# Kernel tuning notes

Measured on AMD Instinct MI355X. Metric: run time of the kernel, lower is better.

The kernel has to match this reference:

```python
import jax, jax.numpy as jnp
import numpy as np

T, F, H = 91, 256, 4
D = F // H  # 64
KF = 4 * F  # FFN hidden
A, R = 128, 1024


def setup_inputs() -> dict:
    key = jax.random.key(0)
    ks = jax.random.split(key, 16)
    s = 1.0 / np.sqrt(F)
    inp = {
        "agent": jax.random.normal(ks[0], (A, T, F), jnp.float32),
        "rg": jax.random.normal(ks[1], (R, T, F), jnp.float32),
        "W_K": jax.random.uniform(ks[2], (F, F), jnp.float32, -s, s),
        "b_K": jnp.zeros((F,), jnp.float32),
        "W_V": jax.random.uniform(ks[3], (F, F), jnp.float32, -s, s),
        "b_V": jnp.zeros((F,), jnp.float32),
        "W_Q": jax.random.uniform(ks[4], (F, F), jnp.float32, -s, s),
        "b_Q": jnp.zeros((F,), jnp.float32),
        "q_scale": jnp.full((D,), 1e-3, jnp.float32),  # ScaleLayer init_value
        "W_Y2": jax.random.uniform(ks[5], (F, F), jnp.float32, -s, s),
        "b_Y2": jnp.zeros((F,), jnp.float32),
        "W_F1": jax.random.uniform(ks[6], (F, KF), jnp.float32, -s, s),
        "b_F1": jnp.zeros((KF,), jnp.float32),
        "W_F2": jax.random.uniform(ks[7], (KF, F), jnp.float32, -1.0 / np.sqrt(KF), 1.0 / np.sqrt(KF)),
        "b_F2": jnp.zeros((F,), jnp.float32),
        "ln_g": jnp.ones((F,), jnp.float32),
        "ln_b": jnp.zeros((F,), jnp.float32),
    }
    return inp


def _proj_heads(x, W, b):
    # Linear + ReLU + View(-1, T, H, D) + permute(1,2,0,3) -> [T, H, N, D]
    y = jax.nn.relu(x @ W + b)                      # [N, T, F]
    y = y.reshape(-1, T, H, D)
    return jnp.transpose(y, (1, 2, 0, 3))            # [T, H, N, D]


def _layernorm(x, g, b, eps=1e-5):
    mu = jnp.mean(x, axis=-1, keepdims=True)
    var = jnp.var(x, axis=-1, keepdims=True)
    return (x - mu) * jax.lax.rsqrt(var + eps) * g + b


def reference(agent, rg, W_K, b_K, W_V, b_V, W_Q, b_Q, q_scale,
              W_Y2, b_Y2, W_F1, b_F1, W_F2, b_F2, ln_g, ln_b):
    Kh = _proj_heads(rg, W_K, b_K)                   # [T, H, R, D]
    Vh = _proj_heads(rg, W_V, b_V)                   # [T, H, R, D]
    Qh = _proj_heads(agent, W_Q, b_Q) * q_scale      # [T, H, A, D] (per-channel scale)

    scale = jnp.sqrt(jnp.asarray(float(H), jnp.float32))  # sqrt(head_num), as in source
    energy = jnp.einsum('thad,thrd->thar', Qh, Kh) / scale
    attn = jax.nn.softmax(energy, axis=-1)           # [T, H, A, R]
    Y1 = jnp.einsum('thar,thrd->thad', attn, Vh)     # [T, H, A, D]
    Y1 = jnp.transpose(Y1, (2, 0, 1, 3)).reshape(-1, T, F)  # [A, T, F]

    Y2 = jax.nn.relu(Y1 @ W_Y2 + b_Y2)               # [A, T, F]
    S = Y2 + agent
    F1 = jax.nn.relu(S @ W_F1 + b_F1)                # [A, T, 4F]
    F2 = jax.nn.relu(F1 @ W_F2 + b_F2)               # [A, T, F]
    Z = _layernorm(F2, ln_g, ln_b)
    return (Z, Qh, Kh, Vh)
```

## Files before the change

### kernel.cpp

```cpp
#include <hip/hip_runtime.h>

#define T91  91
#define FDIM 256
#define HNUM 4
#define DDIM 64
#define ANUM 128
#define RNUM 1024
#define KFDIM 1024

typedef __attribute__((ext_vector_type(8))) short short8v;
typedef __attribute__((ext_vector_type(4))) float f32x4;

__device__ __forceinline__ ushort f2bf(float f) {
  union { float f; uint32_t u; } c; c.f = f;
  return (ushort)((c.u + 0x7FFFu + ((c.u >> 16) & 1u)) >> 16);
}
__device__ __forceinline__ short8v pack8(float4 a, float4 b) {
  short8v v;
  v[0] = (short)f2bf(a.x); v[1] = (short)f2bf(a.y);
  v[2] = (short)f2bf(a.z); v[3] = (short)f2bf(a.w);
  v[4] = (short)f2bf(b.x); v[5] = (short)f2bf(b.y);
  v[6] = (short)f2bf(b.z); v[7] = (short)f2bf(b.w);
  return v;
}

__global__ __launch_bounds__(256) void wconv(
    const float* __restrict__ W, ushort* __restrict__ Wt, int Kd, int Md, int total) {
  const int o = blockIdx.x * 256 + threadIdx.x;
  if (o >= total) return;
  const int m = o / Kd, k = o - m * Kd;
  Wt[o] = f2bf(W[(size_t)k * Md + m]);
}

template<int ISV>
__global__ __launch_bounds__(256) void kvproj_mfma(
    const float* __restrict__ rg, const ushort* __restrict__ Wt,
    const float* __restrict__ bias, float* __restrict__ outKV,
    ushort* __restrict__ Vt) {
  const int rt = blockIdx.x;
  const int tfix = blockIdx.y;
  const int tid = threadIdx.x;
  const int wid = tid >> 6, lane = tid & 63, lg = lane >> 4, li = lane & 15;

  __shared__ ushort As[64 * 64];
  __shared__ ushort Bs[256 * 64];

  const int r0 = rt * 64;
  const int ar = tid >> 2, aseg = (tid & 3) * 16;
  const float* arow = rg + ((size_t)(r0 + ar) * T91 + tfix) * FDIM;

  f32x4 acc[4][4];
  #pragma unroll
  for (int a = 0; a < 4; ++a)
    #pragma unroll
    for (int b = 0; b < 4; ++b)
      #pragma unroll
      for (int i = 0; i < 4; ++i) acc[a][b][i] = 0.f;

  for (int ks = 0; ks < 4; ++ks) {
    const int k0 = ks * 64;
    float4 a0 = *(const float4*)&arow[k0 + aseg + 0];
    float4 a1 = *(const float4*)&arow[k0 + aseg + 4];
    float4 a2 = *(const float4*)&arow[k0 + aseg + 8];
    float4 a3 = *(const float4*)&arow[k0 + aseg + 12];
    short8v bv[8];
    #pragma unroll
    for (int j = 0; j < 8; ++j)
      bv[j] = *(const short8v*)&Wt[(size_t)tid * 256 + k0 + j * 8];
    __syncthreads();
    {
      const int sw = (ar & 7) << 4;
      const int ab = ar * 128 + (tid & 3) * 32;
      *(short8v*)((char*)As + ((ab + 0) ^ sw)) = pack8(a0, a1);
      *(short8v*)((char*)As + ((ab + 16) ^ sw)) = pack8(a2, a3);
      const int swb = (tid & 7) << 4;
      #pragma unroll
      for (int j = 0; j < 8; ++j)
        *(short8v*)((char*)Bs + (tid * 128 + ((j * 16) ^ swb))) = bv[j];
    }
    __syncthreads();
    #pragma unroll
    for (int kc = 0; kc < 2; ++kc) {
      short8v af[4], bfr[4];
      #pragma unroll
      for (int ms = 0; ms < 4; ++ms) {
        const int r = ms * 16 + li;
        af[ms] = *(const short8v*)((char*)As + ((r * 128 + kc * 64 + lg * 16) ^ ((r & 7) << 4)));
      }
      #pragma unroll
      for (int ns = 0; ns < 4; ++ns) {
        const int n = wid * 64 + ns * 16 + li;
        bfr[ns] = *(const short8v*)((char*)Bs + ((n * 128 + kc * 64 + lg * 16) ^ ((n & 7) << 4)));
      }
      #pragma unroll
      for (int ms = 0; ms < 4; ++ms)
        #pragma unroll
        for (int ns = 0; ns < 4; ++ns)
          acc[ms][ns] = __builtin_amdgcn_mfma_f32_16x16x32_bf16(af[ms], bfr[ns], acc[ms][ns], 0, 0, 0);
    }
  }

  const int th = tfix * HNUM + wid;
  float* kout = outKV + (size_t)th * RNUM * DDIM;
  #pragma unroll
  for (int ns = 0; ns < 4; ++ns) {
    const int d = ns * 16 + li;
    const float bb = bias[wid * 64 + d];
    #pragma unroll
    for (int ms = 0; ms < 4; ++ms) {
      float v[4];
      #pragma unroll
      for (int i = 0; i < 4; ++i) {
        v[i] = fmaxf(acc[ms][ns][i] + bb, 0.f);
        kout[(size_t)(r0 + ms * 16 + lg * 4 + i) * DDIM + d] = v[i];
      }
      if (ISV) {
        ushort4 u = {f2bf(v[0]), f2bf(v[1]), f2bf(v[2]), f2bf(v[3])};
        *(ushort4*)&Vt[((size_t)(th * 16 + rt) * 64 + d) * 64 + ms * 16 + lg * 4] = u;
      }
    }
  }
}

template<int MODE>
__global__ __launch_bounds__(256) void mfma_gemm(
    const float* __restrict__ A, const ushort* __restrict__ Wt,
    const float* __restrict__ bias, float* __restrict__ out,
    const float* __restrict__ aux) {
  const int n0 = blockIdx.y * 64;
  const int m0 = blockIdx.x * 256;
  const int tid = threadIdx.x;
  const int wid = tid >> 6, lane = tid & 63, lg = lane >> 4, li = lane & 15;

  __shared__ ushort As[64 * 64];
  __shared__ ushort Bs[256 * 64];

  const int ar = tid >> 2, aseg = (tid & 3) * 16;
  const float* arow = A + (size_t)(n0 + ar) * 256;

  f32x4 acc[4][4];
  #pragma unroll
  for (int a = 0; a < 4; ++a)
    #pragma unroll
    for (int b = 0; b < 4; ++b)
      #pragma unroll
      for (int i = 0; i < 4; ++i) acc[a][b][i] = 0.f;

  for (int ks = 0; ks < 4; ++ks) {
    const int k0 = ks * 64;
    float4 a0 = *(const float4*)&arow[k0 + aseg + 0];
    float4 a1 = *(const float4*)&arow[k0 + aseg + 4];
    float4 a2 = *(const float4*)&arow[k0 + aseg + 8];
    float4 a3 = *(const float4*)&arow[k0 + aseg + 12];
    short8v bv[8];
    #pragma unroll
    for (int j = 0; j < 8; ++j)
      bv[j] = *(const short8v*)&Wt[(size_t)(m0 + tid) * 256 + k0 + j * 8];
    __syncthreads();
    {
      const int sw = (ar & 7) << 4;
      const int ab = ar * 128 + (tid & 3) * 32;
      *(short8v*)((char*)As + ((ab + 0) ^ sw)) = pack8(a0, a1);
      *(short8v*)((char*)As + ((ab + 16) ^ sw)) = pack8(a2, a3);
      const int swb = (tid & 7) << 4;
      #pragma unroll
      for (int j = 0; j < 8; ++j)
        *(short8v*)((char*)Bs + (tid * 128 + ((j * 16) ^ swb))) = bv[j];
    }
    __syncthreads();
    #pragma unroll
    for (int kc = 0; kc < 2; ++kc) {
      short8v af[4], bfr[4];
      #pragma unroll
      for (int ms = 0; ms < 4; ++ms) {
        const int r = ms * 16 + li;
        af[ms] = *(const short8v*)((char*)As + ((r * 128 + kc * 64 + lg * 16) ^ ((r & 7) << 4)));
      }
      #pragma unroll
      for (int ns = 0; ns < 4; ++ns) {
        const int n = wid * 64 + ns * 16 + li;
        bfr[ns] = *(const short8v*)((char*)Bs + ((n * 128 + kc * 64 + lg * 16) ^ ((n & 7) << 4)));
      }
      #pragma unroll
      for (int ms = 0; ms < 4; ++ms)
        #pragma unroll
        for (int ns = 0; ns < 4; ++ns)
          acc[ms][ns] = __builtin_amdgcn_mfma_f32_16x16x32_bf16(af[ms], bfr[ns], acc[ms][ns], 0, 0, 0);
    }
  }

  #pragma unroll
  for (int ns = 0; ns < 4; ++ns) {
    const int c = wid * 64 + ns * 16 + li;
    const float bb = bias[m0 + c];
    float qs = 0.f;
    if (MODE == 0) qs = aux[c & 63];
    #pragma unroll
    for (int ms = 0; ms < 4; ++ms) {
      #pragma unroll
      for (int i = 0; i < 4; ++i) {
        const int n = n0 + ms * 16 + lg * 4 + i;
        float v = fmaxf(acc[ms][ns][i] + bb, 0.f);
        if (MODE == 0) {
          const int a = n / T91, t = n - a * T91;
          out[(((size_t)t * HNUM + (c >> 6)) * ANUM + a) * DDIM + (c & 63)] = v * qs;
        } else if (MODE == 1) {
          out[(size_t)n * FDIM + c] = v + aux[(size_t)n * FDIM + c];
        } else {
          ((ushort*)out)[(size_t)n * KFDIM + m0 + c] = f2bf(v);
        }
      }
    }
  }
}

__global__ __launch_bounds__(512) void f2_ln_mfma(
    const ushort* __restrict__ F1b, const ushort* __restrict__ Wt,
    const float* __restrict__ b2, const float* __restrict__ g,
    const float* __restrict__ bb, float* __restrict__ Z) {
  const int n0 = blockIdx.x * 64;
  const int tid = threadIdx.x;
  const int wid = tid >> 6, lane = tid & 63, lg = lane >> 4, li = lane & 15;

  __shared__ ushort As[64 * 64];
  __shared__ ushort Bs[256 * 64];
  __shared__ float red[64][8][2];

  const int ar = tid >> 3, aseg = tid & 7;
  const int br = tid >> 1, bh = tid & 1;

  f32x4 acc[4][2];
  #pragma unroll
  for (int a = 0; a < 4; ++a)
    #pragma unroll
    for (int b = 0; b < 2; ++b)
      #pragma unroll
      for (int i = 0; i < 4; ++i) acc[a][b][i] = 0.f;

  for (int ks = 0; ks < 16; ++ks) {
    const int k0 = ks * 64;
    short8v av = *(const short8v*)&F1b[(size_t)(n0 + ar) * KFDIM + k0 + aseg * 8];
    short8v bv[4];
    #pragma unroll
    for (int j = 0; j < 4; ++j)
      bv[j] = *(const short8v*)&Wt[(size_t)br * KFDIM + k0 + bh * 32 + j * 8];
    __syncthreads();
    *(short8v*)((char*)As + (ar * 128 + ((aseg * 16) ^ ((ar & 7) << 4)))) = av;
    #pragma unroll
    for (int j = 0; j < 4; ++j)
      *(short8v*)((char*)Bs + (br * 128 + ((bh * 64 + j * 16) ^ ((br & 7) << 4)))) = bv[j];
    __syncthreads();
    #pragma unroll
    for (int kc = 0; kc < 2; ++kc) {
      short8v af[4], bfr[2];
      #pragma unroll
      for (int ms = 0; ms < 4; ++ms) {
        const int r = ms * 16 + li;
        af[ms] = *(const short8v*)((char*)As + ((r * 128 + kc * 64 + lg * 16) ^ ((r & 7) << 4)));
      }
      #pragma unroll
      for (int ns = 0; ns < 2; ++ns) {
        const int n = wid * 32 + ns * 16 + li;
        bfr[ns] = *(const short8v*)((char*)Bs + ((n * 128 + kc * 64 + lg * 16) ^ ((n & 7) << 4)));
      }
      #pragma unroll
      for (int ms = 0; ms < 4; ++ms)
        #pragma unroll
        for (int ns = 0; ns < 2; ++ns)
          acc[ms][ns] = __builtin_amdgcn_mfma_f32_16x16x32_bf16(af[ms], bfr[ns], acc[ms][ns], 0, 0, 0);
    }
  }

  #pragma unroll
  for (int ms = 0; ms < 4; ++ms) {
    #pragma unroll
    for (int i = 0; i < 4; ++i) {
      float s = 0.f, sq = 0.f;
      #pragma unroll
      for (int ns = 0; ns < 2; ++ns) {
        const float b = b2[wid * 32 + ns * 16 + li];
        float v = fmaxf(acc[ms][ns][i] + b, 0.f);
        acc[ms][ns][i] = v;
        s += v; sq += v * v;
      }
      s += __shfl_xor(s, 1); sq += __shfl_xor(sq, 1);
      s += __shfl_xor(s, 2); sq += __shfl_xor(sq, 2);
      s += __shfl_xor(s, 4); sq += __shfl_xor(sq, 4);
      s += __shfl_xor(s, 8); sq += __shfl_xor(sq, 8);
      if (li == 0) {
        const int r = ms * 16 + lg * 4 + i;
        red[r][wid][0] = s; red[r][wid][1] = sq;
      }
    }
  }
  __syncthreads();

  const float g0 = g[wid * 32 + li],       g1 = g[wid * 32 + 16 + li];
  const float e0 = bb[wid * 32 + li],      e1 = bb[wid * 32 + 16 + li];
  #pragma unroll
  for (int ms = 0; ms < 4; ++ms) {
    #pragma unroll
    for (int i = 0; i < 4; ++i) {
      const int r = ms * 16 + lg * 4 + i;
      float s = 0.f, sq = 0.f;
      #pragma unroll
      for (int w = 0; w < 8; ++w) { s += red[r][w][0]; sq += red[r][w][1]; }
      const float mu = s * (1.f / 256.f);
      const float var = sq * (1.f / 256.f) - mu * mu;
      const float rs = rsqrtf(var + 1e-5f);
      float* zp = Z + (size_t)(n0 + r) * FDIM;
      zp[wid * 32 + li]      = (acc[ms][0][i] - mu) * rs * g0 + e0;
      zp[wid * 32 + 16 + li] = (acc[ms][1][i] - mu) * rs * g1 + e1;
    }
  }
}

__global__ __launch_bounds__(256) void attn_mfma(
    const float* __restrict__ Qh, const float* __restrict__ Kh,
    const ushort* __restrict__ Vt, float* __restrict__ Pacc,
    float* __restrict__ Pml) {
  const int th = blockIdx.x, g = blockIdx.y;
  const int tid = threadIdx.x;
  const int wid = tid >> 6, lane = tid & 63;
  const int lg = lane >> 4, li = lane & 15;

  __shared__ ushort Kl[4096];
  __shared__ ushort Vl[4096];
  __shared__ ushort Pl[8192];

  short8v qf[2][2];
  #pragma unroll
  for (int qsub = 0; qsub < 2; ++qsub)
    #pragma unroll
    for (int kc = 0; kc < 2; ++kc) {
      const float* qp = Qh + ((size_t)th * ANUM + wid * 32 + qsub * 16 + li) * DDIM + kc * 32 + lg * 8;
      float4 x = *(const float4*)qp;
      float4 y = *(const float4*)(qp + 4);
      qf[qsub][kc] = pack8(make_float4(x.x*0.5f, x.y*0.5f, x.z*0.5f, x.w*0.5f),
                           make_float4(y.x*0.5f, y.y*0.5f, y.z*0.5f, y.w*0.5f));
    }

  f32x4 yacc[2][4];
  #pragma unroll
  for (int a = 0; a < 2; ++a)
    #pragma unroll
    for (int b = 0; b < 4; ++b)
      #pragma unroll
      for (int i = 0; i < 4; ++i) yacc[a][b][i] = 0.f;

  float mrow[2][4], lrow[2][4];
  #pragma unroll
  for (int a = 0; a < 2; ++a)
    #pragma unroll
    for (int i = 0; i < 4; ++i) { mrow[a][i] = -1e30f; lrow[a][i] = 0.f; }

  const float*  Kb = Kh + (size_t)th * RNUM * DDIM;
  const ushort* Vb = Vt + (size_t)th * 16 * 4096;

  const int krr = wid * 16 + (lane >> 2);
  const int kd0 = (lane & 3) * 16;

  for (int tt = 0; tt < 8; ++tt) {
    const int r0 = g * 512 + tt * 64;
    const int rt = g * 8 + tt;
    __syncthreads();
    {
      const float* kp = Kb + (size_t)(r0 + krr) * DDIM + kd0;
      float4 a = *(const float4*)kp,       b = *(const float4*)(kp + 4),
             c = *(const float4*)(kp + 8), d = *(const float4*)(kp + 12);
      const int base = krr * 128 + kd0 * 2;
      const int sw = (krr & 7) << 4;
      *(short8v*)((char*)Kl + (base ^ sw)) = pack8(a, b);
      *(short8v*)((char*)Kl + ((base + 16) ^ sw)) = pack8(c, d);
    }
    const ushort* vtile = Vb + rt * 4096;
    #pragma unroll
    for (int c = 0; c < 2; ++c) {
      const int B = (wid * 2 + c) * 1024 + lane * 16;
      const int sw = ((B >> 7) & 7) << 4;
      short8v v = *(const short8v*)((const char*)vtile + (B ^ sw));
      *(short8v*)((char*)Vl + B) = v;
    }
    __syncthreads();

    f32x4 sf[2][4];
    #pragma unroll
    for (int a = 0; a < 2; ++a)
      #pragma unroll
      for (int b = 0; b < 4; ++b)
        #pragma unroll
        for (int i = 0; i < 4; ++i) sf[a][b][i] = 0.f;

    #pragma unroll
    for (int kc = 0; kc < 2; ++kc) {
      short8v kf[4];
      #pragma unroll
      for (int rsub = 0; rsub < 4; ++rsub) {
        const int rl = rsub * 16 + li;
        kf[rsub] = *(const short8v*)((char*)Kl + ((rl * 128 + kc * 64 + lg * 16) ^ ((rl & 7) << 4)));
      }
      #pragma unroll
      for (int qsub = 0; qsub < 2; ++qsub)
        #pragma unroll
        for (int rsub = 0; rsub < 4; ++rsub)
          sf[qsub][rsub] = __builtin_amdgcn_mfma_f32_16x16x32_bf16(
              qf[qsub][kc], kf[rsub], sf[qsub][rsub], 0, 0, 0);
    }

    #pragma unroll
    for (int qsub = 0; qsub < 2; ++qsub)
      #pragma unroll
      for (int i = 0; i < 4; ++i) {
        float em = fmaxf(fmaxf(sf[qsub][0][i], sf[qsub][1][i]),
                         fmaxf(sf[qsub][2][i], sf[qsub][3][i]));
        em = fmaxf(em, __shfl_xor(em, 1));
        em = fmaxf(em, __shfl_xor(em, 2));
        em = fmaxf(em, __shfl_xor(em, 4));
        em = fmaxf(em, __shfl_xor(em, 8));
        const float mn = fmaxf(mrow[qsub][i], em);
        const float fs = __expf(mrow[qsub][i] - mn);
        mrow[qsub][i] = mn;
        const float p0 = __expf(sf[qsub][0][i] - mn);
        const float p1 = __expf(sf[qsub][1][i] - mn);
        const float p2 = __expf(sf[qsub][2][i] - mn);
        const float p3 = __expf(sf[qsub][3][i] - mn);
        float rs = p0 + p1 + p2 + p3;
        rs += __shfl_xor(rs, 1);
        rs += __shfl_xor(rs, 2);
        rs += __shfl_xor(rs, 4);
        rs += __shfl_xor(rs, 8);
        lrow[qsub][i] = lrow[qsub][i] * fs + rs;
        #pragma unroll
        for (int dsub = 0; dsub < 4; ++dsub) yacc[qsub][dsub][i] *= fs;
        const int q = qsub * 16 + lg * 4 + i;
        const int sw = (q & 7) << 4;
        char* pb = (char*)Pl + wid * 4096;
        *(ushort*)(pb + ((q * 128 + (0 * 16 + li) * 2) ^ sw)) = f2bf(p0);
        *(ushort*)(pb + ((q * 128 + (1 * 16 + li) * 2) ^ sw)) = f2bf(p1);
        *(ushort*)(pb + ((q * 128 + (2 * 16 + li) * 2) ^ sw)) = f2bf(p2);
        *(ushort*)(pb + ((q * 128 + (3 * 16 + li) * 2) ^ sw)) = f2bf(p3);
      }

    #pragma unroll
    for (int rc = 0; rc < 2; ++rc) {
      short8v pa[2];
      #pragma unroll
      for (int qsub = 0; qsub < 2; ++qsub) {
        const int qq = qsub * 16 + li;
        pa[qsub] = *(const short8v*)((char*)Pl + wid * 4096 +
                    ((qq * 128 + rc * 64 + lg * 16) ^ ((qq & 7) << 4)));
      }
      #pragma unroll
      for (int dsub = 0; dsub < 4; ++dsub) {
        const int dd = dsub * 16 + li;
        short8v vb = *(const short8v*)((char*)Vl +
                      ((dd * 128 + rc * 64 + lg * 16) ^ ((dd & 7) << 4)));
        #pragma unroll
        for (int qsub = 0; qsub < 2; ++qsub)
          yacc[qsub][dsub] = __builtin_amdgcn_mfma_f32_16x16x32_bf16(
              pa[qsub], vb, yacc[qsub][dsub], 0, 0, 0);
      }
    }
  }

  const int thg = th * 2 + g;
  float* pp = Pacc + (size_t)thg * 8192;
  #pragma unroll
  for (int qsub = 0; qsub < 2; ++qsub)
    #pragma unroll
    for (int dsub = 0; dsub < 4; ++dsub)
      #pragma unroll
      for (int i = 0; i < 4; ++i) {
        const int q = wid * 32 + qsub * 16 + lg * 4 + i;
        pp[q * 64 + dsub * 16 + li] = yacc[qsub][dsub][i];
      }
  if (li == 0) {
    #pragma unroll
    for (int qsub = 0; qsub < 2; ++qsub)
      #pragma unroll
      for (int i = 0; i < 4; ++i) {
        const int q = wid * 32 + qsub * 16 + lg * 4 + i;
        Pml[(size_t)thg * 256 + q] = mrow[qsub][i];
        Pml[(size_t)thg * 256 + 128 + q] = lrow[qsub][i];
      }
  }
}

__global__ __launch_bounds__(128) void attn_combine(
    const float* __restrict__ Pacc, const float* __restrict__ Pml,
    float* __restrict__ Y1) {
  const int th = blockIdx.x;
  const int t = th >> 2, h = th & 3;
  const int a = threadIdx.x;
  const float m0 = Pml[(size_t)(th * 2 + 0) * 256 + a];
  const float l0 = Pml[(size_t)(th * 2 + 0) * 256 + 128 + a];
  const float m1 = Pml[(size_t)(th * 2 + 1) * 256 + a];
  const float l1 = Pml[(size_t)(th * 2 + 1) * 256 + 128 + a];
  const float mn = fmaxf(m0, m1);
  const float s0 = __expf(m0 - mn), s1 = __expf(m1 - mn);
  const float inv = 1.f / (s0 * l0 + s1 * l1);
  const float* p0 = Pacc + (size_t)(th * 2 + 0) * 8192 + a * 64;
  const float* p1 = Pacc + (size_t)(th * 2 + 1) * 8192 + a * 64;
  float* yp = Y1 + ((size_t)a * T91 + t) * FDIM + h * DDIM;
  #pragma unroll
  for (int i = 0; i < 16; ++i) {
    float4 v0 = *(const float4*)(p0 + i * 4);
    float4 v1 = *(const float4*)(p1 + i * 4);
    float4 o = {(s0 * v0.x + s1 * v1.x) * inv, (s0 * v0.y + s1 * v1.y) * inv,
                (s0 * v0.z + s1 * v1.z) * inv, (s0 * v0.w + s1 * v1.w) * inv};
    *(float4*)(yp + i * 4) = o;
  }
}

extern "C" void kernel_launch(void* const* d_in, const int* in_sizes, int n_in,
                              void* d_out, int out_size, void* d_ws, size_t ws_size,
                              hipStream_t stream) {
  (void)in_sizes; (void)n_in; (void)out_size; (void)ws_size;

  const float* agent   = (const float*)d_in[0];
  const float* rg      = (const float*)d_in[1];
  const float* W_K     = (const float*)d_in[2];
  const float* b_K     = (const float*)d_in[3];
  const float* W_V     = (const float*)d_in[4];
  const float* b_V     = (const float*)d_in[5];
  const float* W_Q     = (const float*)d_in[6];
  const float* b_Q     = (const float*)d_in[7];
  const float* q_scale = (const float*)d_in[8];
  const float* W_Y2    = (const float*)d_in[9];
  const float* b_Y2    = (const float*)d_in[10];
  const float* W_F1    = (const float*)d_in[11];
  const float* b_F1    = (const float*)d_in[12];
  const float* W_F2    = (const float*)d_in[13];
  const float* b_F2    = (const float*)d_in[14];
  const float* ln_g    = (const float*)d_in[15];
  const float* ln_b    = (const float*)d_in[16];

  float* out = (float*)d_out;
  float* Z  = out;
  float* Qh = out + 2981888;
  float* Kh = out + 5963776;
  float* Vh = out + 29818880;

  char* w = (char*)d_ws;
  ushort* WKt  = (ushort*)w;                    w += 65536 * 2;
  ushort* WVt  = (ushort*)w;                    w += 65536 * 2;
  ushort* WQt  = (ushort*)w;                    w += 65536 * 2;
  ushort* WY2t = (ushort*)w;                    w += 65536 * 2;
  ushort* WF1t = (ushort*)w;                    w += 262144 * 2;
  ushort* WF2t = (ushort*)w;                    w += 262144 * 2;
  float*  S    = (float*)w;                     w += (size_t)11648 * 256 * 4;
  ushort* F1b  = (ushort*)w;                    w += (size_t)11648 * 1024 * 2;
  ushort* Vt   = (ushort*)w;
  float*  Y1   = (float*)Vt;
  float*  Pacc = (float*)F1b;
  float*  Pml  = S;

  const dim3 blk(256);

  wconv<<<dim3(256), blk, 0, stream>>>(W_K,  WKt,  256, 256, 65536);
  wconv<<<dim3(256), blk, 0, stream>>>(W_V,  WVt,  256, 256, 65536);
  wconv<<<dim3(256), blk, 0, stream>>>(W_Q,  WQt,  256, 256, 65536);
  wconv<<<dim3(256), blk, 0, stream>>>(W_Y2, WY2t, 256, 256, 65536);
  wconv<<<dim3(1024), blk, 0, stream>>>(W_F1, WF1t, 256, 1024, 262144);
  wconv<<<dim3(1024), blk, 0, stream>>>(W_F2, WF2t, 1024, 256, 262144);

  kvproj_mfma<0><<<dim3(16, 91), blk, 0, stream>>>(rg, WKt, b_K, Kh, nullptr);
  kvproj_mfma<1><<<dim3(16, 91), blk, 0, stream>>>(rg, WVt, b_V, Vh, Vt);
  mfma_gemm<0><<<dim3(1, 182), blk, 0, stream>>>(agent, WQt, b_Q, Qh, q_scale);

  attn_mfma<<<dim3(364, 2), blk, 0, stream>>>(Qh, Kh, Vt, Pacc, Pml);
  attn_combine<<<dim3(364), dim3(128), 0, stream>>>(Pacc, Pml, Y1);

  mfma_gemm<1><<<dim3(1, 182), blk, 0, stream>>>(Y1, WY2t, b_Y2, S, agent);
  mfma_gemm<2><<<dim3(4, 182), blk, 0, stream>>>(S, WF1t, b_F1, (float*)F1b, nullptr);
  f2_ln_mfma<<<dim3(182), dim3(512), 0, stream>>>(F1b, WF2t, b_F2, ln_g, ln_b, Z);
}
```

Measured before the change: 557.0 us.

## Fuse weight conversions, K/V projections, and attention combine into Y2 GEMM

Merges the six weight-conversion launches into one kernel and fuses the K and V projections into a single 512-thread kernel, so each rg tile is loaded once for both. Removes the attn_combine kernel and the Y1 round trip by having the Y2 GEMM merge the two attention partials (m/l rescaling) while loading its A tile. Computes attention scores transposed so each lane owns one query row, which turns most cross-lane softmax shuffles into in-register reductions, and packs P to bf16 with v_cvt_pk_bf16_f32. The fused K/V kernel uses more LDS and threads per block, which may lower occupancy, and Pml moves to its own workspace region.

```diff
diff --git a/kernel.cpp b/kernel.cpp
--- a/kernel.cpp
+++ b/kernel.cpp
@@ -23,31 +23,53 @@
   v[6] = (short)f2bf(b.z); v[7] = (short)f2bf(b.w);
   return v;
 }
-
-__global__ __launch_bounds__(256) void wconv(
-    const float* __restrict__ W, ushort* __restrict__ Wt, int Kd, int Md, int total) {
-  const int o = blockIdx.x * 256 + threadIdx.x;
-  if (o >= total) return;
+__device__ __forceinline__ uint32_t cvtpk(float lo, float hi) {
+  uint32_t r;
+  asm("v_cvt_pk_bf16_f32 %0, %1, %2" : "=v"(r) : "v"(lo), "v"(hi));
+  return r;
+}
+
+__global__ __launch_bounds__(256) void wconv_all(
+    const float* __restrict__ W_K, const float* __restrict__ W_V,
+    const float* __restrict__ W_Q, const float* __restrict__ W_Y2,
+    const float* __restrict__ W_F1, const float* __restrict__ W_F2,
+    ushort* __restrict__ WKt, ushort* __restrict__ WVt,
+    ushort* __restrict__ WQt, ushort* __restrict__ WY2t,
+    ushort* __restrict__ WF1t, ushort* __restrict__ WF2t) {
+  const int b = blockIdx.x, tid = threadIdx.x;
+  const float* W; ushort* Wt; int Kd, Md, o;
+  if (b < 1024) {
+    const int s = b >> 8;
+    W  = (s == 0) ? W_K : (s == 1) ? W_V : (s == 2) ? W_Q : W_Y2;
+    Wt = (s == 0) ? WKt : (s == 1) ? WVt : (s == 2) ? WQt : WY2t;
+    Kd = 256; Md = 256; o = (b & 255) * 256 + tid;
+  } else if (b < 2048) {
+    W = W_F1; Wt = WF1t; Kd = 256; Md = 1024; o = (b - 1024) * 256 + tid;
+  } else {
+    W = W_F2; Wt = WF2t; Kd = 1024; Md = 256; o = (b - 2048) * 256 + tid;
+  }
   const int m = o / Kd, k = o - m * Kd;
   Wt[o] = f2bf(W[(size_t)k * Md + m]);
 }
 
-template<int ISV>
-__global__ __launch_bounds__(256) void kvproj_mfma(
-    const float* __restrict__ rg, const ushort* __restrict__ Wt,
-    const float* __restrict__ bias, float* __restrict__ outKV,
-    ushort* __restrict__ Vt) {
+__global__ __launch_bounds__(512) void kvproj_fused(
+    const float* __restrict__ rg, const ushort* __restrict__ WKt,
+    const ushort* __restrict__ WVt, const float* __restrict__ b_K,
+    const float* __restrict__ b_V, float* __restrict__ Kh,
+    float* __restrict__ Vh, ushort* __restrict__ Vt) {
   const int rt = blockIdx.x;
   const int tfix = blockIdx.y;
   const int tid = threadIdx.x;
   const int wid = tid >> 6, lane = tid & 63, lg = lane >> 4, li = lane & 15;
 
   __shared__ ushort As[64 * 64];
-  __shared__ ushort Bs[256 * 64];
+  __shared__ ushort Bs[512 * 64];
 
   const int r0 = rt * 64;
-  const int ar = tid >> 2, aseg = (tid & 3) * 16;
+  const int ar = tid >> 3, aseg = (tid & 7) * 8;
   const float* arow = rg + ((size_t)(r0 + ar) * T91 + tfix) * FDIM;
+  const ushort* brow = (tid < 256) ? (WKt + (size_t)tid * 256)
+                                   : (WVt + (size_t)(tid - 256) * 256);
 
   f32x4 acc[4][4];
   #pragma unroll
@@ -61,18 +83,14 @@
     const int k0 = ks * 64;
     float4 a0 = *(const float4*)&arow[k0 + aseg + 0];
     float4 a1 = *(const float4*)&arow[k0 + aseg + 4];
-    float4 a2 = *(const float4*)&arow[k0 + aseg + 8];
-    float4 a3 = *(const float4*)&arow[k0 + aseg + 12];
     short8v bv[8];
     #pragma unroll
     for (int j = 0; j < 8; ++j)
-      bv[j] = *(const short8v*)&Wt[(size_t)tid * 256 + k0 + j * 8];
+      bv[j] = *(const short8v*)&brow[k0 + j * 8];
     __syncthreads();
     {
       const int sw = (ar & 7) << 4;
-      const int ab = ar * 128 + (tid & 3) * 32;
-      *(short8v*)((char*)As + ((ab + 0) ^ sw)) = pack8(a0, a1);
-      *(short8v*)((char*)As + ((ab + 16) ^ sw)) = pack8(a2, a3);
+      *(short8v*)((char*)As + (ar * 128 + (((tid & 7) * 16) ^ sw))) = pack8(a0, a1);
       const int swb = (tid & 7) << 4;
       #pragma unroll
       for (int j = 0; j < 8; ++j)
@@ -100,12 +118,15 @@
     }
   }
 
-  const int th = tfix * HNUM + wid;
-  float* kout = outKV + (size_t)th * RNUM * DDIM;
+  const int hsel = wid & 3;
+  const int th = tfix * HNUM + hsel;
+  const bool isv = wid >= 4;
+  const float* bias = isv ? b_V : b_K;
+  float* kout = (isv ? Vh : Kh) + (size_t)th * RNUM * DDIM;
   #pragma unroll
   for (int ns = 0; ns < 4; ++ns) {
     const int d = ns * 16 + li;
-    const float bb = bias[wid * 64 + d];
+    const float bb = bias[hsel * 64 + d];
     #pragma unroll
     for (int ms = 0; ms < 4; ++ms) {
       float v[4];
@@ -114,7 +135,7 @@
         v[i] = fmaxf(acc[ms][ns][i] + bb, 0.f);
         kout[(size_t)(r0 + ms * 16 + lg * 4 + i) * DDIM + d] = v[i];
       }
-      if (ISV) {
+      if (isv) {
         ushort4 u = {f2bf(v[0]), f2bf(v[1]), f2bf(v[2]), f2bf(v[3])};
         *(ushort4*)&Vt[((size_t)(th * 16 + rt) * 64 + d) * 64 + ms * 16 + lg * 4] = u;
       }
@@ -204,11 +225,105 @@
         if (MODE == 0) {
           const int a = n / T91, t = n - a * T91;
           out[(((size_t)t * HNUM + (c >> 6)) * ANUM + a) * DDIM + (c & 63)] = v * qs;
-        } else if (MODE == 1) {
-          out[(size_t)n * FDIM + c] = v + aux[(size_t)n * FDIM + c];
         } else {
           ((ushort*)out)[(size_t)n * KFDIM + m0 + c] = f2bf(v);
         }
+      }
+    }
+  }
+}
+
+__global__ __launch_bounds__(256) void y2_gemm(
+    const float* __restrict__ Pacc, const float* __restrict__ Pml,
+    const ushort* __restrict__ Wt, const float* __restrict__ bias,
+    float* __restrict__ S, const float* __restrict__ agent) {
+  const int n0 = blockIdx.x * 64;
+  const int tid = threadIdx.x;
+  const int wid = tid >> 6, lane = tid & 63, lg = lane >> 4, li = lane & 15;
+
+  __shared__ ushort As[64 * 64];
+  __shared__ ushort Bs[256 * 64];
+
+  const int ar = tid >> 2, aseg = (tid & 3) * 16;
+  const int n = n0 + ar;
+  const int a = n / T91, t = n - a * T91;
+
+  f32x4 acc[4][4];
+  #pragma unroll
+  for (int q = 0; q < 4; ++q)
+    #pragma unroll
+    for (int b = 0; b < 4; ++b)
+      #pragma unroll
+      for (int i = 0; i < 4; ++i) acc[q][b][i] = 0.f;
+
+  for (int ks = 0; ks < 4; ++ks) {
+    const int k0 = ks * 64;
+    const int th = t * 4 + ks;
+    const float m0v = Pml[(size_t)(th * 2 + 0) * 256 + a];
+    const float l0v = Pml[(size_t)(th * 2 + 0) * 256 + 128 + a];
+    const float m1v = Pml[(size_t)(th * 2 + 1) * 256 + a];
+    const float l1v = Pml[(size_t)(th * 2 + 1) * 256 + 128 + a];
+    const float mn = fmaxf(m0v, m1v);
+    const float s0 = __expf(m0v - mn), s1 = __expf(m1v - mn);
+    const float inv = 1.f / (s0 * l0v + s1 * l1v);
+    const float* p0 = Pacc + (size_t)(th * 2 + 0) * 8192 + a * 64 + aseg;
+    const float* p1 = Pacc + (size_t)(th * 2 + 1) * 8192 + a * 64 + aseg;
+    float4 x[4];
+    #pragma unroll
+    for (int j = 0; j < 4; ++j) {
+      float4 u = *(const float4*)(p0 + j * 4);
+      float4 v = *(const float4*)(p1 + j * 4);
+      x[j] = make_float4((s0 * u.x + s1 * v.x) * inv, (s0 * u.y + s1 * v.y) * inv,
+                         (s0 * u.z + s1 * v.z) * inv, (s0 * u.w + s1 * v.w) * inv);
+    }
+    short8v bv[8];
+    #pragma unroll
+    for (int j = 0; j < 8; ++j)
+      bv[j] = *(const short8v*)&Wt[(size_t)tid * 256 + k0 + j * 8];
+    __syncthreads();
+    {
+      const int sw = (ar & 7) << 4;
+      const int ab = ar * 128 + (tid & 3) * 32;
+      *(short8v*)((char*)As + ((ab + 0) ^ sw)) = pack8(x[0], x[1]);
+      *(short8v*)((char*)As + ((ab + 16) ^ sw)) = pack8(x[2], x[3]);
+      const int swb = (tid & 7) << 4;
+      #pragma unroll
+      for (int j = 0; j < 8; ++j)
+        *(short8v*)((char*)Bs + (tid * 128 + ((j * 16) ^ swb))) = bv[j];
+    }
+    __syncthreads();
+    #pragma unroll
+    for (int kc = 0; kc < 2; ++kc) {
+      short8v af[4], bfr[4];
+      #pragma unroll
+      for (int ms = 0; ms < 4; ++ms) {
+        const int r = ms * 16 + li;
+        af[ms] = *(const short8v*)((char*)As + ((r * 128 + kc * 64 + lg * 16) ^ ((r & 7) << 4)));
+      }
+      #pragma unroll
+      for (int ns = 0; ns < 4; ++ns) {
+        const int nn = wid * 64 + ns * 16 + li;
+        bfr[ns] = *(const short8v*)((char*)Bs + ((nn * 128 + kc * 64 + lg * 16) ^ ((nn & 7) << 4)));
+      }
+      #pragma unroll
+      for (int ms = 0; ms < 4; ++ms)
+        #pragma unroll
+        for (int ns = 0; ns < 4; ++ns)
+          acc[ms][ns] = __builtin_amdgcn_mfma_f32_16x16x32_bf16(af[ms], bfr[ns], acc[ms][ns], 0, 0, 0);
+    }
+  }
+
+  #pragma unroll
+  for (int ns = 0; ns < 4; ++ns) {
+    const int c = wid * 64 + ns * 16 + li;
+    const float bb = bias[c];
+    #pragma unroll
+    for (int ms = 0; ms < 4; ++ms) {
+      #pragma unroll
+      for (int i = 0; i < 4; ++i) {
+        const int nn = n0 + ms * 16 + lg * 4 + i;
+        float v = fmaxf(acc[ms][ns][i] + bb, 0.f);
+        S[(size_t)nn * FDIM + c] = v + agent[(size_t)nn * FDIM + c];
       }
     }
   }
@@ -340,19 +455,15 @@
                            make_float4(y.x*0.5f, y.y*0.5f, y.z*0.5f, y.w*0.5f));
     }
 
-  f32x4 yacc[2][4];
+  f32x4 yaccT[2][4];
   #pragma unroll
   for (int a = 0; a < 2; ++a)
     #pragma unroll
     for (int b = 0; b < 4; ++b)
       #pragma unroll
-      for (int i = 0; i < 4; ++i) yacc[a][b][i] = 0.f;
-
-  float mrow[2][4], lrow[2][4];
-  #pragma unroll
-  for (int a = 0; a < 2; ++a)
-    #pragma unroll
-    for (int i = 0; i < 4; ++i) { mrow[a][i] = -1e30f; lrow[a][i] = 0.f; }
+      for (int i = 0; i < 4; ++i) yaccT[a][b][i] = 0.f;
+
+  float mq[2] = {-1e30f, -1e30f}, lq[2] = {0.f, 0.f};
 
   const float*  Kb = Kh + (size_t)th * RNUM * DDIM;
   const ushort* Vb = Vt + (size_t)th * 16 * 4096;
@@ -383,13 +494,13 @@
     }
     __syncthreads();
 
-    f32x4 sf[2][4];
+    f32x4 sfT[2][4];
     #pragma unroll
     for (int a = 0; a < 2; ++a)
       #pragma unroll
       for (int b = 0; b < 4; ++b)
         #pragma unroll
-        for (int i = 0; i < 4; ++i) sf[a][b][i] = 0.f;
+        for (int i = 0; i < 4; ++i) sfT[a][b][i] = 0.f;
 
     #pragma unroll
     for (int kc = 0; kc < 2; ++kc) {
@@ -403,52 +514,58 @@
       for (int qsub = 0; qsub < 2; ++qsub)
         #pragma unroll
         for (int rsub = 0; rsub < 4; ++rsub)
-          sf[qsub][rsub] = __builtin_amdgcn_mfma_f32_16x16x32_bf16(
-              qf[qsub][kc], kf[rsub], sf[qsub][rsub], 0, 0, 0);
-    }
-
-    #pragma unroll
-    for (int qsub = 0; qsub < 2; ++qsub)
-      #pragma unroll
-      for (int i = 0; i < 4; ++i) {
-        float em = fmaxf(fmaxf(sf[qsub][0][i], sf[qsub][1][i]),
-                         fmaxf(sf[qsub][2][i], sf[qsub][3][i]));
-        em = fmaxf(em, __shfl_xor(em, 1));
-        em = fmaxf(em, __shfl_xor(em, 2));
-        em = fmaxf(em, __shfl_xor(em, 4));
-        em = fmaxf(em, __shfl_xor(em, 8));
-        const float mn = fmaxf(mrow[qsub][i], em);
-        const float fs = __expf(mrow[qsub][i] - mn);
-        mrow[qsub][i] = mn;
-        const float p0 = __expf(sf[qsub][0][i] - mn);
-        const float p1 = __expf(sf[qsub][1][i] - mn);
-        const float p2 = __expf(sf[qsub][2][i] - mn);
-        const float p3 = __expf(sf[qsub][3][i] - mn);
-        float rs = p0 + p1 + p2 + p3;
-        rs += __shfl_xor(rs, 1);
-        rs += __shfl_xor(rs, 2);
-        rs += __shfl_xor(rs, 4);
-        rs += __shfl_xor(rs, 8);
-        lrow[qsub][i] = lrow[qsub][i] * fs + rs;
-        #pragma unroll
-        for (int dsub = 0; dsub < 4; ++dsub) yacc[qsub][dsub][i] *= fs;
-        const int q = qsub * 16 + lg * 4 + i;
-        const int sw = (q & 7) << 4;
-        char* pb = (char*)Pl + wid * 4096;
-        *(ushort*)(pb + ((q * 128 + (0 * 16 + li) * 2) ^ sw)) = f2bf(p0);
-        *(ushort*)(pb + ((q * 128 + (1 * 16 + li) * 2) ^ sw)) = f2bf(p1);
-        *(ushort*)(pb + ((q * 128 + (2 * 16 + li) * 2) ^ sw)) = f2bf(p2);
-        *(ushort*)(pb + ((q * 128 + (3 * 16 + li) * 2) ^ sw)) = f2bf(p3);
-      }
+          sfT[qsub][rsub] = __builtin_amdgcn_mfma_f32_16x16x32_bf16(
+              kf[rsub], qf[qsub][kc], sfT[qsub][rsub], 0, 0, 0);
+    }
+
+    #pragma unroll
+    for (int qsub = 0; qsub < 2; ++qsub) {
+      float em = sfT[qsub][0][0];
+      #pragma unroll
+      for (int rsub = 0; rsub < 4; ++rsub)
+        #pragma unroll
+        for (int i = 0; i < 4; ++i)
+          em = fmaxf(em, sfT[qsub][rsub][i]);
+      em = fmaxf(em, __shfl_xor(em, 16));
+      em = fmaxf(em, __shfl_xor(em, 32));
+      const float mn = fmaxf(mq[qsub], em);
+      const float fs = __expf(mq[qsub] - mn);
+      mq[qsub] = mn;
+      float rs = 0.f;
+      #pragma unroll
+      for (int rsub = 0; rsub < 4; ++rsub)
+        #pragma unroll
+        for (int i = 0; i < 4; ++i) {
+          const float p = __expf(sfT[qsub][rsub][i] - mn);
+          sfT[qsub][rsub][i] = p;
+          rs += p;
+        }
+      rs += __shfl_xor(rs, 16);
+      rs += __shfl_xor(rs, 32);
+      lq[qsub] = lq[qsub] * fs + rs;
+      #pragma unroll
+      for (int dsub = 0; dsub < 4; ++dsub)
+        #pragma unroll
+        for (int i = 0; i < 4; ++i) yaccT[qsub][dsub][i] *= fs;
+      const int qloc = qsub * 16 + li;
+      const int sw = (qloc & 7) << 4;
+      char* pb = (char*)Pl + wid * 4096;
+      #pragma unroll
+      for (int rsub = 0; rsub < 4; ++rsub) {
+        uint2 cc = {cvtpk(sfT[qsub][rsub][0], sfT[qsub][rsub][1]),
+                    cvtpk(sfT[qsub][rsub][2], sfT[qsub][rsub][3])};
+        *(uint2*)(pb + (qloc * 128 + ((rsub * 32 + lg * 8) ^ sw))) = cc;
+      }
+    }
 
     #pragma unroll
     for (int rc = 0; rc < 2; ++rc) {
-      short8v pa[2];
+      short8v pbf[2];
       #pragma unroll
       for (int qsub = 0; qsub < 2; ++qsub) {
-        const int qq = qsub * 16 + li;
-        pa[qsub] = *(const short8v*)((char*)Pl + wid * 4096 +
-                    ((qq * 128 + rc * 64 + lg * 16) ^ ((qq & 7) << 4)));
+        const int qloc = qsub * 16 + li;
+        pbf[qsub] = *(const short8v*)((char*)Pl + wid * 4096 +
+                     (qloc * 128 + ((rc * 64 + lg * 16) ^ ((qloc & 7) << 4))));
       }
       #pragma unroll
       for (int dsub = 0; dsub < 4; ++dsub) {
@@ -457,8 +574,8 @@
                       ((dd * 128 + rc * 64 + lg * 16) ^ ((dd & 7) << 4)));
         #pragma unroll
         for (int qsub = 0; qsub < 2; ++qsub)
-          yacc[qsub][dsub] = __builtin_amdgcn_mfma_f32_16x16x32_bf16(
-              pa[qsub], vb, yacc[qsub][dsub], 0, 0, 0);
+          yaccT[qsub][dsub] = __builtin_amdgcn_mfma_f32_16x16x32_bf16(
+              vb, pbf[qsub], yaccT[qsub][dsub], 0, 0, 0);
       }
     }
   }
@@ -466,49 +583,18 @@
   const int thg = th * 2 + g;
   float* pp = Pacc + (size_t)thg * 8192;
   #pragma unroll
-  for (int qsub = 0; qsub < 2; ++qsub)
-    #pragma unroll
-    for (int dsub = 0; dsub < 4; ++dsub)
-      #pragma unroll
-      for (int i = 0; i < 4; ++i) {
-        const int q = wid * 32 + qsub * 16 + lg * 4 + i;
-        pp[q * 64 + dsub * 16 + li] = yacc[qsub][dsub][i];
-      }
-  if (li == 0) {
-    #pragma unroll
-    for (int qsub = 0; qsub < 2; ++qsub)
-      #pragma unroll
-      for (int i = 0; i < 4; ++i) {
-        const int q = wid * 32 + qsub * 16 + lg * 4 + i;
-        Pml[(size_t)thg * 256 + q] = mrow[qsub][i];
-        Pml[(size_t)thg * 256 + 128 + q] = lrow[qsub][i];
-      }
-  }
-}
-
-__global__ __launch_bounds__(128) void attn_combine(
-    const float* __restrict__ Pacc, const float* __restrict__ Pml,
-    float* __restrict__ Y1) {
-  const int th = blockIdx.x;
-  const int t = th >> 2, h = th & 3;
-  const int a = threadIdx.x;
-  const float m0 = Pml[(size_t)(th * 2 + 0) * 256 + a];
-  const float l0 = Pml[(size_t)(th * 2 + 0) * 256 + 128 + a];
-  const float m1 = Pml[(size_t)(th * 2 + 1) * 256 + a];
-  const float l1 = Pml[(size_t)(th * 2 + 1) * 256 + 128 + a];
-  const float mn = fmaxf(m0, m1);
-  const float s0 = __expf(m0 - mn), s1 = __expf(m1 - mn);
-  const float inv = 1.f / (s0 * l0 + s1 * l1);
-  const float* p0 = Pacc + (size_t)(th * 2 + 0) * 8192 + a * 64;
-  const float* p1 = Pacc + (size_t)(th * 2 + 1) * 8192 + a * 64;
-  float* yp = Y1 + ((size_t)a * T91 + t) * FDIM + h * DDIM;
-  #pragma unroll
-  for (int i = 0; i < 16; ++i) {
-    float4 v0 = *(const float4*)(p0 + i * 4);
-    float4 v1 = *(const float4*)(p1 + i * 4);
-    float4 o = {(s0 * v0.x + s1 * v1.x) * inv, (s0 * v0.y + s1 * v1.y) * inv,
-                (s0 * v0.z + s1 * v1.z) * inv, (s0 * v0.w + s1 * v1.w) * inv};
-    *(float4*)(yp + i * 4) = o;
+  for (int qsub = 0; qsub < 2; ++qsub) {
+    const int q = wid * 32 + qsub * 16 + li;
+    #pragma unroll
+    for (int dsub = 0; dsub < 4; ++dsub) {
+      float4 o = {yaccT[qsub][dsub][0], yaccT[qsub][dsub][1],
+                  yaccT[qsub][dsub][2], yaccT[qsub][dsub][3]};
+      *(float4*)&pp[q * 64 + dsub * 16 + lg * 4] = o;
+    }
+    if (lg == 0) {
+      Pml[(size_t)thg * 256 + q] = mq[qsub];
+      Pml[(size_t)thg * 256 + 128 + q] = lq[qsub];
+    }
   }
 }
 
@@ -549,29 +635,22 @@
   ushort* WF1t = (ushort*)w;                    w += 262144 * 2;
   ushort* WF2t = (ushort*)w;                    w += 262144 * 2;
   float*  S    = (float*)w;                     w += (size_t)11648 * 256 * 4;
+  float*  Pml  = (float*)w;                     w += (size_t)728 * 256 * 4;
   ushort* F1b  = (ushort*)w;                    w += (size_t)11648 * 1024 * 2;
   ushort* Vt   = (ushort*)w;
-  float*  Y1   = (float*)Vt;
   float*  Pacc = (float*)F1b;
-  float*  Pml  = S;
 
   const dim3 blk(256);
 
-  wconv<<<dim3(256), blk, 0, stream>>>(W_K,  WKt,  256, 256, 65536);
-  wconv<<<dim3(256), blk, 0, stream>>>(W_V,  WVt,  256, 256, 65536);
-  wconv<<<dim3(256), blk, 0, stream>>>(W_Q,  WQt,  256, 256, 65536);
-  wconv<<<dim3(256), blk, 0, stream>>>(W_Y2, WY2t, 256, 256, 65536);
-  wconv<<<dim3(1024), blk, 0, stream>>>(W_F1, WF1t, 256, 1024, 262144);
-  wconv<<<dim3(1024), blk, 0, stream>>>(W_F2, WF2t, 1024, 256, 262144);
-
-  kvproj_mfma<0><<<dim3(16, 91), blk, 0, stream>>>(rg, WKt, b_K, Kh, nullptr);
-  kvproj_mfma<1><<<dim3(16, 91), blk, 0, stream>>>(rg, WVt, b_V, Vh, Vt);
+  wconv_all<<<dim3(3072), blk, 0, stream>>>(W_K, W_V, W_Q, W_Y2, W_F1, W_F2,
+                                            WKt, WVt, WQt, WY2t, WF1t, WF2t);
+
+  kvproj_fused<<<dim3(16, 91), dim3(512), 0, stream>>>(rg, WKt, WVt, b_K, b_V, Kh, Vh, Vt);
   mfma_gemm<0><<<dim3(1, 182), blk, 0, stream>>>(agent, WQt, b_Q, Qh, q_scale);
 
   attn_mfma<<<dim3(364, 2), blk, 0, stream>>>(Qh, Kh, Vt, Pacc, Pml);
-  attn_combine<<<dim3(364), dim3(128), 0, stream>>>(Pacc, Pml, Y1);
-
-  mfma_gemm<1><<<dim3(1, 182), blk, 0, stream>>>(Y1, WY2t, b_Y2, S, agent);
+
+  y2_gemm<<<dim3(182), blk, 0, stream>>>(Pacc, Pml, WY2t, b_Y2, S, agent);
   mfma_gemm<2><<<dim3(4, 182), blk, 0, stream>>>(S, WF1t, b_F1, (float*)F1b, nullptr);
   f2_ln_mfma<<<dim3(182), dim3(512), 0, stream>>>(F1b, WF2t, b_F2, ln_g, ln_b, Z);
 }
```

After: 524.3 us. 1.06x faster.
